# Optimization experiments

Hardware: AMD Instinct MI355X
Metric: run time of the kernel (lower is better)

Reference implementation:

```python
import jax, jax.numpy as jnp
import numpy as np
from jax import lax

WINDOW_SIZE = 11
SIGMA = 1.5
DATA_RANGE = 1.0


def gaussian_window(size, sigma):
    k = jnp.arange(size, dtype=jnp.float32) - size // 2
    k = jnp.exp(-0.5 / sigma ** 2 * k ** 2)
    return k / k.sum()


def depthwise_conv(x, window):
    # x: [B,C,H,W], window: [C,1,k,k]
    pad = WINDOW_SIZE // 2
    return lax.conv_general_dilated(
        x, window,
        window_strides=(1, 1),
        padding=[(pad, pad), (pad, pad)],
        dimension_numbers=('NCHW', 'OIHW', 'NCHW'),
        feature_group_count=x.shape[1])


def setup_inputs() -> dict:
    key = jax.random.key(0)
    k1, k2 = jax.random.split(key)
    img1 = jax.random.uniform(k1, (32, 3, 512, 512), dtype=jnp.float32)
    img2 = jax.random.uniform(k2, (32, 3, 512, 512), dtype=jnp.float32)
    return {"img1": img1, "img2": img2}


def reference(img1, img2):
    channels = img1.shape[1]
    w1 = gaussian_window(WINDOW_SIZE, SIGMA)[:, None]        # [k,1]
    w2 = w1 @ w1.T                                           # [k,k]
    window = jnp.broadcast_to(w2, (channels, 1, WINDOW_SIZE, WINDOW_SIZE))

    C1 = (0.01 * DATA_RANGE) ** 2
    C2 = (0.03 * DATA_RANGE) ** 2

    mu1 = depthwise_conv(img1, window)
    mu2 = depthwise_conv(img2, window)
    mu1_sq = mu1 * mu1
    mu2_sq = mu2 * mu2
    mu1_mu2 = mu1 * mu2
    sigma1_sq = depthwise_conv(img1 * img1, window) - mu1_sq
    sigma2_sq = depthwise_conv(img2 * img2, window) - mu2_sq
    sigma12 = depthwise_conv(img1 * img2, window) - mu1_mu2

    ssim_map = ((2 * mu1_mu2 + C1) * (2 * sigma12 + C2)) / (
        (mu1_sq + mu2_sq + C1) * (sigma1_sq + sigma2_sq + C2))
    return 1.0 - ssim_map.mean()
```

## Files before the change

### kernel.cpp

```cpp
#include <hip/hip_runtime.h>
#include <math.h>

#define TX 128
#define TY 32
#define TXH 138
#define TXP 148
#define NTHREADS 512

constexpr int H = 512, W = 512;
constexpr int NPLANES = 96;
constexpr int GX = W / TX;
constexpr int GY = H / TY;
constexpr int NB = GX * GY * NPLANES;
constexpr double NTOT = 25165824.0;
constexpr float C1 = 1.0e-4f;
constexpr float C2 = 9.0e-4f;

struct Wts { float w[11]; };

template<bool EDGE>
__device__ __forceinline__ void phase1(const float* __restrict__ p1,
                                       const float* __restrict__ p2,
                                       float (&vb)[4][TY][TXP],
                                       int tx0, int ty0, const Wts& wts, int tid)
{
    for (int i = tid; i < (TY / 4) * TXH; i += NTHREADS) {
        const int rh = i / TXH;
        const int c  = i - rh * TXH;
        const int x  = tx0 - 5 + c;
        const int yb = ty0 - 5 + 4 * rh;
        const bool xin = (x >= 0) && (x < W);

        float aA[4]  = {0.f, 0.f, 0.f, 0.f};
        float aB[4]  = {0.f, 0.f, 0.f, 0.f};
        float aQa[4] = {0.f, 0.f, 0.f, 0.f};
        float aQb[4] = {0.f, 0.f, 0.f, 0.f};

        #pragma unroll
        for (int t = 0; t < 14; ++t) {
            const int y = yb + t;
            float v1 = 0.f, v2 = 0.f;
            if (EDGE) {
                if (xin && (y >= 0) && (y < H)) {
                    v1 = p1[y * W + x];
                    v2 = p2[y * W + x];
                }
            } else {
                v1 = p1[y * W + x];
                v2 = p2[y * W + x];
            }
            const float av = v1 + v2, bv = v1 - v2;
            const float a2 = av * av, b2 = bv * bv;
            #pragma unroll
            for (int d = 0; d < 4; ++d) {
                const int k = t - d;
                if (k >= 0 && k <= 10) {
                    const float wk = wts.w[k];
                    aA[d]  = fmaf(wk, av, aA[d]);
                    aB[d]  = fmaf(wk, bv, aB[d]);
                    aQa[d] = fmaf(wk, a2, aQa[d]);
                    aQb[d] = fmaf(wk, b2, aQb[d]);
                }
            }
        }
        #pragma unroll
        for (int d = 0; d < 4; ++d) {
            const int r = 4 * rh + d;
            vb[0][r][c] = aA[d];
            vb[1][r][c] = aB[d];
            vb[2][r][c] = aQa[d];
            vb[3][r][c] = aQb[d];
        }
    }
}

__global__ __launch_bounds__(NTHREADS, 4)
void ssim_main_kernel(const float* __restrict__ img1, const float* __restrict__ img2,
                      float* __restrict__ part, Wts wts)
{
    __shared__ float vb[4][TY][TXP];
    __shared__ float red[NTHREADS / 64];

    const int tid = threadIdx.x;
    const int tx0 = blockIdx.x * TX;
    const int ty0 = blockIdx.y * TY;
    const long plane = (long)blockIdx.z * (H * W);
    const float* p1 = img1 + plane;
    const float* p2 = img2 + plane;

    const bool edge = (blockIdx.x == 0) || (blockIdx.x == GX - 1) ||
                      (blockIdx.y == 0) || (blockIdx.y == GY - 1);
    if (edge) phase1<true>(p1, p2, vb, tx0, ty0, wts, tid);
    else      phase1<false>(p1, p2, vb, tx0, ty0, wts, tid);

    __syncthreads();

    const int row = tid & 31;
    const int cg  = tid >> 5;
    const int c0  = cg * 8;

    float res[4][8];
    #pragma unroll
    for (int ch = 0; ch < 4; ++ch) {
        float f[20];
        #pragma unroll
        for (int j = 0; j < 5; ++j) {
            const float4 v = *(const float4*)&vb[ch][row][c0 + 4 * j];
            f[4 * j + 0] = v.x; f[4 * j + 1] = v.y;
            f[4 * j + 2] = v.z; f[4 * j + 3] = v.w;
        }
        #pragma unroll
        for (int j = 0; j < 8; ++j) {
            float s = wts.w[0] * f[j];
            #pragma unroll
            for (int k = 1; k < 11; ++k) s = fmaf(wts.w[k], f[j + k], s);
            res[ch][j] = s;
        }
    }

    float local = 0.f;
    #pragma unroll
    for (int j = 0; j < 8; ++j) {
        const float A  = res[0][j], Bv = res[1][j];
        const float Qa = res[2][j], Qb = res[3][j];
        const float u = A * A, v = Bv * Bv;
        const float t1 = u - v;
        const float t2 = u + v;
        const float num1 = fmaf(0.5f, t1, C1);
        const float den1 = fmaf(0.5f, t2, C1);
        const float num2 = fmaf(0.5f, (Qa - Qb) - t1, C2);
        const float den2 = fmaf(0.5f, (Qa + Qb) - t2, C2);
        const float num = num1 * num2;
        const float den = den1 * den2;
        local += num * __builtin_amdgcn_rcpf(den);
    }

    #pragma unroll
    for (int off = 32; off > 0; off >>= 1) local += __shfl_down(local, off, 64);
    if ((tid & 63) == 0) red[tid >> 6] = local;
    __syncthreads();
    if (tid == 0) {
        float s = 0.f;
        #pragma unroll
        for (int wv = 0; wv < NTHREADS / 64; ++wv) s += red[wv];
        const int bid = (blockIdx.z * GY + blockIdx.y) * GX + blockIdx.x;
        part[bid] = s;
    }
}

__global__ __launch_bounds__(512)
void ssim_final_kernel(const float* __restrict__ part, float* __restrict__ out)
{
    __shared__ double red[8];
    const int tid = threadIdx.x;
    double s = 0.0;
    for (int i = tid; i < NB; i += 512) s += (double)part[i];
    #pragma unroll
    for (int off = 32; off > 0; off >>= 1) s += __shfl_down(s, off, 64);
    if ((tid & 63) == 0) red[tid >> 6] = s;
    __syncthreads();
    if (tid == 0) {
        double t = 0.0;
        #pragma unroll
        for (int wv = 0; wv < 8; ++wv) t += red[wv];
        out[0] = (float)(1.0 - t / NTOT);
    }
}

extern "C" void kernel_launch(void* const* d_in, const int* in_sizes, int n_in,
                              void* d_out, int out_size, void* d_ws, size_t ws_size,
                              hipStream_t stream)
{
    const float* img1 = (const float*)d_in[0];
    const float* img2 = (const float*)d_in[1];
    float* out = (float*)d_out;
    float* part = (float*)d_ws;

    Wts wts;
    double wd[11], s = 0.0;
    for (int k = 0; k < 11; ++k) {
        const double d = (double)(k - 5);
        wd[k] = exp(-0.5 / (1.5 * 1.5) * d * d);
        s += wd[k];
    }
    for (int k = 0; k < 11; ++k) wts.w[k] = (float)(wd[k] / s);

    dim3 grid(GX, GY, NPLANES);
    ssim_main_kernel<<<grid, NTHREADS, 0, stream>>>(img1, img2, part, wts);
    ssim_final_kernel<<<1, 512, 0, stream>>>(part, out);
}
```

Measured before the change: 271.0 us.

## Compute separable Gaussian convolutions as fp16 MFMA banded-matrix products

Replaces the scalar FMA vertical and horizontal 11-tap passes with MFMA 16x16x32 fp16 matrix multiplies against a banded Toeplitz weight matrix held in shared memory. Inputs and their squares are converted to fp16 and staged transposed in LDS. Tiles shrink to 64x16 with 256 threads, and the final reduction uses 1024 threads. This moves the convolution work from vector ALUs onto the matrix cores, at the cost of fp16 precision for the intermediates (squared terms and variances), which could break accuracy tolerance.

```diff
diff --git a/kernel.cpp b/kernel.cpp
--- a/kernel.cpp
+++ b/kernel.cpp
@@ -1,13 +1,15 @@
 #include <hip/hip_runtime.h>
 #include <math.h>
 
-#define TX 128
-#define TY 32
-#define TXH 138
-#define TXP 148
-#define NTHREADS 512
+typedef _Float16 f16;
+typedef f16 f16x8 __attribute__((ext_vector_type(8)));
+typedef f16 f16x2 __attribute__((ext_vector_type(2)));
+typedef float f32x4 __attribute__((ext_vector_type(4)));
+
+#define NTHREADS 256
 
 constexpr int H = 512, W = 512;
+constexpr int TX = 64, TY = 16;
 constexpr int NPLANES = 96;
 constexpr int GX = W / TX;
 constexpr int GY = H / TY;
@@ -16,113 +18,124 @@
 constexpr float C1 = 1.0e-4f;
 constexpr float C2 = 9.0e-4f;
 
+constexpr int PRE_COLS = 80;
+constexpr int PRE_RP   = 40;
+constexpr int VC_P     = 88;
+
 struct Wts { float w[11]; };
 
-template<bool EDGE>
-__device__ __forceinline__ void phase1(const float* __restrict__ p1,
-                                       const float* __restrict__ p2,
-                                       float (&vb)[4][TY][TXP],
-                                       int tx0, int ty0, const Wts& wts, int tid)
-{
-    for (int i = tid; i < (TY / 4) * TXH; i += NTHREADS) {
-        const int rh = i / TXH;
-        const int c  = i - rh * TXH;
-        const int x  = tx0 - 5 + c;
-        const int yb = ty0 - 5 + 4 * rh;
-        const bool xin = (x >= 0) && (x < W);
-
-        float aA[4]  = {0.f, 0.f, 0.f, 0.f};
-        float aB[4]  = {0.f, 0.f, 0.f, 0.f};
-        float aQa[4] = {0.f, 0.f, 0.f, 0.f};
-        float aQb[4] = {0.f, 0.f, 0.f, 0.f};
-
-        #pragma unroll
-        for (int t = 0; t < 14; ++t) {
-            const int y = yb + t;
-            float v1 = 0.f, v2 = 0.f;
-            if (EDGE) {
-                if (xin && (y >= 0) && (y < H)) {
-                    v1 = p1[y * W + x];
-                    v2 = p2[y * W + x];
-                }
-            } else {
-                v1 = p1[y * W + x];
-                v2 = p2[y * W + x];
-            }
-            const float av = v1 + v2, bv = v1 - v2;
-            const float a2 = av * av, b2 = bv * bv;
-            #pragma unroll
-            for (int d = 0; d < 4; ++d) {
-                const int k = t - d;
-                if (k >= 0 && k <= 10) {
-                    const float wk = wts.w[k];
-                    aA[d]  = fmaf(wk, av, aA[d]);
-                    aB[d]  = fmaf(wk, bv, aB[d]);
-                    aQa[d] = fmaf(wk, a2, aQa[d]);
-                    aQb[d] = fmaf(wk, b2, aQb[d]);
-                }
-            }
-        }
-        #pragma unroll
-        for (int d = 0; d < 4; ++d) {
-            const int r = 4 * rh + d;
-            vb[0][r][c] = aA[d];
-            vb[1][r][c] = aB[d];
-            vb[2][r][c] = aQa[d];
-            vb[3][r][c] = aQb[d];
-        }
-    }
+__device__ __forceinline__ void store_pre(f16 (&preS)[4][PRE_COLS][PRE_RP],
+                                          int c, int rp,
+                                          float v1a, float v1b, float v2a, float v2b)
+{
+    const float A0 = v1a + v2a, B0 = v1a - v2a;
+    const float A1 = v1b + v2b, B1 = v1b - v2b;
+    f16x2 hA  = { (f16)A0,        (f16)A1 };
+    f16x2 hB  = { (f16)B0,        (f16)B1 };
+    f16x2 hQa = { (f16)(A0 * A0), (f16)(A1 * A1) };
+    f16x2 hQb = { (f16)(B0 * B0), (f16)(B1 * B1) };
+    *(f16x2*)&preS[0][c][2 * rp] = hA;
+    *(f16x2*)&preS[1][c][2 * rp] = hB;
+    *(f16x2*)&preS[2][c][2 * rp] = hQa;
+    *(f16x2*)&preS[3][c][2 * rp] = hQb;
 }
 
 __global__ __launch_bounds__(NTHREADS, 4)
-void ssim_main_kernel(const float* __restrict__ img1, const float* __restrict__ img2,
-                      float* __restrict__ part, Wts wts)
-{
-    __shared__ float vb[4][TY][TXP];
-    __shared__ float red[NTHREADS / 64];
+void ssim_main(const float* __restrict__ img1, const float* __restrict__ img2,
+               float* __restrict__ part, Wts wts)
+{
+    __shared__ __align__(16) f16 preS[4][PRE_COLS][PRE_RP];
+    __shared__ __align__(16) f16 vcS[4][16][VC_P];
+    __shared__ __align__(16) f16 TbS[16][40];
+    __shared__ float red[4];
 
     const int tid = threadIdx.x;
     const int tx0 = blockIdx.x * TX;
     const int ty0 = blockIdx.y * TY;
-    const long plane = (long)blockIdx.z * (H * W);
+    const size_t plane = (size_t)blockIdx.z * (size_t)(H * W);
     const float* p1 = img1 + plane;
     const float* p2 = img2 + plane;
 
+    for (int i = tid; i < 512; i += NTHREADS) {
+        const int m = i >> 5, k = i & 31, d = k - m;
+        TbS[m][k] = (d >= 0 && d <= 10) ? (f16)wts.w[d] : (f16)0.0f;
+    }
+
     const bool edge = (blockIdx.x == 0) || (blockIdx.x == GX - 1) ||
                       (blockIdx.y == 0) || (blockIdx.y == GY - 1);
-    if (edge) phase1<true>(p1, p2, vb, tx0, ty0, wts, tid);
-    else      phase1<false>(p1, p2, vb, tx0, ty0, wts, tid);
-
-    __syncthreads();
-
-    const int row = tid & 31;
-    const int cg  = tid >> 5;
-    const int c0  = cg * 8;
-
-    float res[4][8];
-    #pragma unroll
-    for (int ch = 0; ch < 4; ++ch) {
-        float f[20];
-        #pragma unroll
-        for (int j = 0; j < 5; ++j) {
-            const float4 v = *(const float4*)&vb[ch][row][c0 + 4 * j];
-            f[4 * j + 0] = v.x; f[4 * j + 1] = v.y;
-            f[4 * j + 2] = v.z; f[4 * j + 3] = v.w;
+
+    if (!edge) {
+        #pragma unroll
+        for (int t = 0; t < 5; ++t) {
+            const int i  = t * NTHREADS + tid;
+            const int c  = i % PRE_COLS;
+            const int rp = i / PRE_COLS;
+            const bool valid = (c < 74) & (rp < 13);
+            const int x = tx0 - 5 + c;
+            const int y = ty0 - 5 + 2 * rp;
+            float v1a = 0.f, v1b = 0.f, v2a = 0.f, v2b = 0.f;
+            if (valid) {
+                const float* q1 = p1 + y * W + x;
+                const float* q2 = p2 + y * W + x;
+                v1a = q1[0]; v1b = q1[W];
+                v2a = q2[0]; v2b = q2[W];
+            }
+            store_pre(preS, c, rp, v1a, v1b, v2a, v2b);
         }
-        #pragma unroll
-        for (int j = 0; j < 8; ++j) {
-            float s = wts.w[0] * f[j];
+    } else {
+        #pragma unroll
+        for (int t = 0; t < 5; ++t) {
+            const int i  = t * NTHREADS + tid;
+            const int c  = i % PRE_COLS;
+            const int rp = i / PRE_COLS;
+            const int x = tx0 - 5 + c;
+            const int y = ty0 - 5 + 2 * rp;
+            const bool cv = (c < 74) && (rp < 13) && (x >= 0) && (x < W);
+            float v1a = 0.f, v1b = 0.f, v2a = 0.f, v2b = 0.f;
+            if (cv && y >= 0 && y < H)         { v1a = p1[y * W + x];       v2a = p2[y * W + x]; }
+            if (cv && y + 1 >= 0 && y + 1 < H) { v1b = p1[(y + 1) * W + x]; v2b = p2[(y + 1) * W + x]; }
+            store_pre(preS, c, rp, v1a, v1b, v2a, v2b);
+        }
+    }
+    __syncthreads();
+
+    const int lane = tid & 63;
+    const int wave = tid >> 6;
+    const int tr = lane & 15;
+    const int k0 = (lane >> 4) * 8;
+    const int m0 = (lane >> 4) * 4;
+
+    const f16x8 aT = *(const f16x8*)&TbS[tr][k0];
+    const f32x4 zero4 = { 0.f, 0.f, 0.f, 0.f };
+
+    {
+        const int ch = wave;
+        #pragma unroll
+        for (int cg = 0; cg < 5; ++cg) {
+            const f16x8 bf = *(const f16x8*)&preS[ch][cg * 16 + tr][k0];
+            const f32x4 d = __builtin_amdgcn_mfma_f32_16x16x32_f16(aT, bf, zero4, 0, 0, 0);
+            const int col = cg * 16 + tr;
             #pragma unroll
-            for (int k = 1; k < 11; ++k) s = fmaf(wts.w[k], f[j + k], s);
-            res[ch][j] = s;
+            for (int i2 = 0; i2 < 4; ++i2)
+                vcS[ch][m0 + i2][col] = (f16)d[i2];
         }
+    }
+    __syncthreads();
+
+    f32x4 r0, r1, r2, r3;
+    {
+        const int G = wave;
+        r0 = __builtin_amdgcn_mfma_f32_16x16x32_f16(aT, *(const f16x8*)&vcS[0][tr][G * 16 + k0], zero4, 0, 0, 0);
+        r1 = __builtin_amdgcn_mfma_f32_16x16x32_f16(aT, *(const f16x8*)&vcS[1][tr][G * 16 + k0], zero4, 0, 0, 0);
+        r2 = __builtin_amdgcn_mfma_f32_16x16x32_f16(aT, *(const f16x8*)&vcS[2][tr][G * 16 + k0], zero4, 0, 0, 0);
+        r3 = __builtin_amdgcn_mfma_f32_16x16x32_f16(aT, *(const f16x8*)&vcS[3][tr][G * 16 + k0], zero4, 0, 0, 0);
     }
 
     float local = 0.f;
     #pragma unroll
-    for (int j = 0; j < 8; ++j) {
-        const float A  = res[0][j], Bv = res[1][j];
-        const float Qa = res[2][j], Qb = res[3][j];
+    for (int i2 = 0; i2 < 4; ++i2) {
+        const float A  = r0[i2], Bv = r1[i2];
+        const float Qa = r2[i2], Qb = r3[i2];
         const float u = A * A, v = Bv * Bv;
         const float t1 = u - v;
         const float t2 = u + v;
@@ -130,31 +143,27 @@
         const float den1 = fmaf(0.5f, t2, C1);
         const float num2 = fmaf(0.5f, (Qa - Qb) - t1, C2);
         const float den2 = fmaf(0.5f, (Qa + Qb) - t2, C2);
-        const float num = num1 * num2;
-        const float den = den1 * den2;
-        local += num * __builtin_amdgcn_rcpf(den);
+        local += (num1 * num2) * __builtin_amdgcn_rcpf(den1 * den2);
     }
 
     #pragma unroll
     for (int off = 32; off > 0; off >>= 1) local += __shfl_down(local, off, 64);
-    if ((tid & 63) == 0) red[tid >> 6] = local;
+    if (lane == 0) red[wave] = local;
     __syncthreads();
     if (tid == 0) {
-        float s = 0.f;
-        #pragma unroll
-        for (int wv = 0; wv < NTHREADS / 64; ++wv) s += red[wv];
+        const float s = red[0] + red[1] + red[2] + red[3];
         const int bid = (blockIdx.z * GY + blockIdx.y) * GX + blockIdx.x;
         part[bid] = s;
     }
 }
 
-__global__ __launch_bounds__(512)
-void ssim_final_kernel(const float* __restrict__ part, float* __restrict__ out)
-{
-    __shared__ double red[8];
+__global__ __launch_bounds__(1024)
+void ssim_final(const float* __restrict__ part, float* __restrict__ out)
+{
+    __shared__ double red[16];
     const int tid = threadIdx.x;
     double s = 0.0;
-    for (int i = tid; i < NB; i += 512) s += (double)part[i];
+    for (int i = tid; i < NB; i += 1024) s += (double)part[i];
     #pragma unroll
     for (int off = 32; off > 0; off >>= 1) s += __shfl_down(s, off, 64);
     if ((tid & 63) == 0) red[tid >> 6] = s;
@@ -162,7 +171,7 @@
     if (tid == 0) {
         double t = 0.0;
         #pragma unroll
-        for (int wv = 0; wv < 8; ++wv) t += red[wv];
+        for (int w = 0; w < 16; ++w) t += red[w];
         out[0] = (float)(1.0 - t / NTOT);
     }
 }
@@ -186,6 +195,6 @@
     for (int k = 0; k < 11; ++k) wts.w[k] = (float)(wd[k] / s);
 
     dim3 grid(GX, GY, NPLANES);
-    ssim_main_kernel<<<grid, NTHREADS, 0, stream>>>(img1, img2, part, wts);
-    ssim_final_kernel<<<1, 512, 0, stream>>>(part, out);
-}
+    ssim_main<<<grid, NTHREADS, 0, stream>>>(img1, img2, part, wts);
+    ssim_final<<<1, 1024, 0, stream>>>(part, out);
+}
```

Measured after the change: 293.6 us. 1.08x slower.

## Use full-width row bands with packed fp16 LDS intermediates and float2 math

Applied to the files above, without the earlier changes.

Each block now handles a full-width band of 16 rows instead of a 128x32 tile, with one thread per column doing the vertical 11-tap pass. The vertical sums (a+b, a-b and their squares) are packed into fp16 pairs in LDS, which halves shared-memory traffic. Both passes use float2 vector arithmetic so the compiler can emit packed FMAs. The band layout cuts horizontal halo work but raises the vertical halo ratio. Rounding the intermediates to fp16 with round-toward-zero (cvt_pkrtz) adds error to the variance terms, which are formed by subtracting nearly equal values.

```diff
diff --git a/kernel.cpp b/kernel.cpp
--- a/kernel.cpp
+++ b/kernel.cpp
@@ -1,138 +1,140 @@
 #include <hip/hip_runtime.h>
 #include <math.h>
 
-#define TX 128
-#define TY 32
-#define TXH 138
-#define TXP 148
+typedef float float2v __attribute__((ext_vector_type(2)));
+typedef unsigned int u32;
+typedef u32 u32x4 __attribute__((ext_vector_type(4)));
+typedef _Float16 f16;
+typedef f16 f16x2 __attribute__((ext_vector_type(2)));
+
 #define NTHREADS 512
 
 constexpr int H = 512, W = 512;
+constexpr int TY = 16;
+constexpr int NBANDS = H / TY;
 constexpr int NPLANES = 96;
-constexpr int GX = W / TX;
-constexpr int GY = H / TY;
-constexpr int NB = GX * GY * NPLANES;
+constexpr int NB = NBANDS * NPLANES;
+constexpr int PITCH = 524;
+constexpr int PAIR = 16 * PITCH;
 constexpr double NTOT = 25165824.0;
 constexpr float C1 = 1.0e-4f;
 constexpr float C2 = 9.0e-4f;
 
 struct Wts { float w[11]; };
 
+__device__ __forceinline__ float2v up2(u32 w) {
+    const f16x2 h = __builtin_bit_cast(f16x2, w);
+    return (float2v){(float)h.x, (float)h.y};
+}
+
 template<bool EDGE>
-__device__ __forceinline__ void phase1(const float* __restrict__ p1,
-                                       const float* __restrict__ p2,
-                                       float (&vb)[4][TY][TXP],
-                                       int tx0, int ty0, const Wts& wts, int tid)
+__device__ __forceinline__ void do_column(const float* __restrict__ p1,
+                                          const float* __restrict__ p2,
+                                          u32* __restrict__ vc,
+                                          const Wts& wts, int cc, int y0)
 {
-    for (int i = tid; i < (TY / 4) * TXH; i += NTHREADS) {
-        const int rh = i / TXH;
-        const int c  = i - rh * TXH;
-        const int x  = tx0 - 5 + c;
-        const int yb = ty0 - 5 + 4 * rh;
-        const bool xin = (x >= 0) && (x < W);
-
-        float aA[4]  = {0.f, 0.f, 0.f, 0.f};
-        float aB[4]  = {0.f, 0.f, 0.f, 0.f};
-        float aQa[4] = {0.f, 0.f, 0.f, 0.f};
-        float aQb[4] = {0.f, 0.f, 0.f, 0.f};
-
+    const int x = cc - 5;
+    const bool xok = (x >= 0) && (x < W);
+    float2v ab[26], qq[26];
+    #pragma unroll
+    for (int t = 0; t < 26; ++t) {
+        const int y = y0 - 5 + t;
+        bool ok = xok;
+        if (EDGE) ok = ok && (y >= 0) && (y < H);
+        const float v1 = ok ? p1[y * W + x] : 0.f;
+        const float v2 = ok ? p2[y * W + x] : 0.f;
+        ab[t] = (float2v){v1 + v2, v1 - v2};
+        qq[t] = ab[t] * ab[t];
+    }
+    u32* wp = vc + cc;
+    #pragma unroll
+    for (int r = 0; r < 16; ++r) {
+        float2v sP = ab[r] * wts.w[0];
+        float2v sQ = qq[r] * wts.w[0];
         #pragma unroll
-        for (int t = 0; t < 14; ++t) {
-            const int y = yb + t;
-            float v1 = 0.f, v2 = 0.f;
-            if (EDGE) {
-                if (xin && (y >= 0) && (y < H)) {
-                    v1 = p1[y * W + x];
-                    v2 = p2[y * W + x];
-                }
-            } else {
-                v1 = p1[y * W + x];
-                v2 = p2[y * W + x];
-            }
-            const float av = v1 + v2, bv = v1 - v2;
-            const float a2 = av * av, b2 = bv * bv;
-            #pragma unroll
-            for (int d = 0; d < 4; ++d) {
-                const int k = t - d;
-                if (k >= 0 && k <= 10) {
-                    const float wk = wts.w[k];
-                    aA[d]  = fmaf(wk, av, aA[d]);
-                    aB[d]  = fmaf(wk, bv, aB[d]);
-                    aQa[d] = fmaf(wk, a2, aQa[d]);
-                    aQb[d] = fmaf(wk, b2, aQb[d]);
-                }
-            }
+        for (int k = 1; k < 11; ++k) {
+            sP += ab[r + k] * wts.w[k];
+            sQ += qq[r + k] * wts.w[k];
         }
-        #pragma unroll
-        for (int d = 0; d < 4; ++d) {
-            const int r = 4 * rh + d;
-            vb[0][r][c] = aA[d];
-            vb[1][r][c] = aB[d];
-            vb[2][r][c] = aQa[d];
-            vb[3][r][c] = aQb[d];
-        }
+        wp[r * PITCH]        = __builtin_bit_cast(u32, __builtin_amdgcn_cvt_pkrtz(sP.x, sP.y));
+        wp[r * PITCH + PAIR] = __builtin_bit_cast(u32, __builtin_amdgcn_cvt_pkrtz(sQ.x, sQ.y));
     }
 }
 
 __global__ __launch_bounds__(NTHREADS, 4)
-void ssim_main_kernel(const float* __restrict__ img1, const float* __restrict__ img2,
-                      float* __restrict__ part, Wts wts)
+void ssim_main(const float* __restrict__ img1, const float* __restrict__ img2,
+               float* __restrict__ part, Wts wts)
 {
-    __shared__ float vb[4][TY][TXP];
-    __shared__ float red[NTHREADS / 64];
+    __shared__ __align__(16) u32 vc[2 * 16 * PITCH];
+    __shared__ float red[8];
 
-    const int tid = threadIdx.x;
-    const int tx0 = blockIdx.x * TX;
-    const int ty0 = blockIdx.y * TY;
-    const long plane = (long)blockIdx.z * (H * W);
+    const int tid  = threadIdx.x;
+    const int band = blockIdx.x;
+    const int y0   = band * TY;
+    const size_t plane = (size_t)blockIdx.y * (size_t)(H * W);
     const float* p1 = img1 + plane;
     const float* p2 = img2 + plane;
 
-    const bool edge = (blockIdx.x == 0) || (blockIdx.x == GX - 1) ||
-                      (blockIdx.y == 0) || (blockIdx.y == GY - 1);
-    if (edge) phase1<true>(p1, p2, vb, tx0, ty0, wts, tid);
-    else      phase1<false>(p1, p2, vb, tx0, ty0, wts, tid);
-
+    if (band == 0 || band == NBANDS - 1) {
+        do_column<true>(p1, p2, vc, wts, tid, y0);
+        if (tid < 10) do_column<true>(p1, p2, vc, wts, 512 + tid, y0);
+    } else {
+        do_column<false>(p1, p2, vc, wts, tid, y0);
+        if (tid < 10) do_column<false>(p1, p2, vc, wts, 512 + tid, y0);
+    }
     __syncthreads();
 
-    const int row = tid & 31;
-    const int cg  = tid >> 5;
-    const int c0  = cg * 8;
+    const int r = tid & 15;
+    const int G = tid >> 4;
+    const u32* row0 = vc + r * PITCH + 16 * G;
 
-    float res[4][8];
+    float2v AB[26];
     #pragma unroll
-    for (int ch = 0; ch < 4; ++ch) {
-        float f[20];
+    for (int i = 0; i < 7; ++i) {
+        const u32x4 t4 = ((const u32x4*)row0)[i];
         #pragma unroll
-        for (int j = 0; j < 5; ++j) {
-            const float4 v = *(const float4*)&vb[ch][row][c0 + 4 * j];
-            f[4 * j + 0] = v.x; f[4 * j + 1] = v.y;
-            f[4 * j + 2] = v.z; f[4 * j + 3] = v.w;
+        for (int e = 0; e < 4; ++e) {
+            const int idx = 4 * i + e;
+            if (idx < 26) AB[idx] = up2(t4[e]);
         }
+    }
+    float2v P[16];
+    #pragma unroll
+    for (int j = 0; j < 16; ++j) {
+        float2v s = AB[j] * wts.w[0];
         #pragma unroll
-        for (int j = 0; j < 8; ++j) {
-            float s = wts.w[0] * f[j];
-            #pragma unroll
-            for (int k = 1; k < 11; ++k) s = fmaf(wts.w[k], f[j + k], s);
-            res[ch][j] = s;
+        for (int k = 1; k < 11; ++k) s += AB[j + k] * wts.w[k];
+        P[j] = s;
+    }
+
+    const u32* row1 = row0 + PAIR;
+    float2v QQ[26];
+    #pragma unroll
+    for (int i = 0; i < 7; ++i) {
+        const u32x4 t4 = ((const u32x4*)row1)[i];
+        #pragma unroll
+        for (int e = 0; e < 4; ++e) {
+            const int idx = 4 * i + e;
+            if (idx < 26) QQ[idx] = up2(t4[e]);
         }
     }
 
     float local = 0.f;
     #pragma unroll
-    for (int j = 0; j < 8; ++j) {
-        const float A  = res[0][j], Bv = res[1][j];
-        const float Qa = res[2][j], Qb = res[3][j];
-        const float u = A * A, v = Bv * Bv;
+    for (int j = 0; j < 16; ++j) {
+        float2v sq = QQ[j] * wts.w[0];
+        #pragma unroll
+        for (int k = 1; k < 11; ++k) sq += QQ[j + k] * wts.w[k];
+        const float A  = P[j].x, B = P[j].y;
+        const float Qa = sq.x,  Qb = sq.y;
+        const float u = A * A, v = B * B;
         const float t1 = u - v;
         const float t2 = u + v;
         const float num1 = fmaf(0.5f, t1, C1);
         const float den1 = fmaf(0.5f, t2, C1);
         const float num2 = fmaf(0.5f, (Qa - Qb) - t1, C2);
         const float den2 = fmaf(0.5f, (Qa + Qb) - t2, C2);
-        const float num = num1 * num2;
-        const float den = den1 * den2;
-        local += num * __builtin_amdgcn_rcpf(den);
+        local += (num1 * num2) * __builtin_amdgcn_rcpf(den1 * den2);
     }
 
     #pragma unroll
@@ -142,14 +144,13 @@
     if (tid == 0) {
         float s = 0.f;
         #pragma unroll
-        for (int wv = 0; wv < NTHREADS / 64; ++wv) s += red[wv];
-        const int bid = (blockIdx.z * GY + blockIdx.y) * GX + blockIdx.x;
-        part[bid] = s;
+        for (int wv = 0; wv < 8; ++wv) s += red[wv];
+        part[blockIdx.y * NBANDS + band] = s;
     }
 }
 
 __global__ __launch_bounds__(512)
-void ssim_final_kernel(const float* __restrict__ part, float* __restrict__ out)
+void ssim_final(const float* __restrict__ part, float* __restrict__ out)
 {
     __shared__ double red[8];
     const int tid = threadIdx.x;
@@ -185,7 +186,7 @@
     }
     for (int k = 0; k < 11; ++k) wts.w[k] = (float)(wd[k] / s);
 
-    dim3 grid(GX, GY, NPLANES);
-    ssim_main_kernel<<<grid, NTHREADS, 0, stream>>>(img1, img2, part, wts);
-    ssim_final_kernel<<<1, 512, 0, stream>>>(part, out);
+    dim3 grid(NBANDS, NPLANES);
+    ssim_main<<<grid, NTHREADS, 0, stream>>>(img1, img2, part, wts);
+    ssim_final<<<1, 512, 0, stream>>>(part, out);
 }
```

After: 242.5 us. 1.12x faster.
